# Optimization experiments

Measured on AMD Instinct MI355X. Metric: run time of the kernel, lower is better.

The kernel has to match this reference:

```python
import jax, jax.numpy as jnp
import numpy as np

N, E, G = 50000, 800000, 1000
F, FM, L, H, T = 128, 16, 7, 128, 12
DIN, DH = 2 * F + 1, 2 * (2 * F + 1)  # 257, 514
UIN, UH = F + FM, 2 * F               # 144, 256

def swish(x):
    return x * jax.nn.sigmoid(x)

def setup_inputs() -> dict:
    key = jax.random.key(0)
    ks = jax.random.split(key, 16)
    pos = jax.random.normal(ks[0], (N, 3), dtype=jnp.float32)
    zi = jax.random.randint(ks[1], (N,), 0, 5)
    z = jnp.array([1, 6, 7, 8, 9], dtype=jnp.int64)[zi]  # valid atomic numbers
    edge_index = jax.random.randint(ks[2], (2, E), 0, N)
    batch = jnp.sort(jax.random.randint(ks[3], (N,), 0, G))
    def w(k, shape, fan_in):
        return jax.random.normal(k, shape, dtype=jnp.float32) / np.sqrt(fan_in)
    return {
        'pos': pos, 'z': z, 'edge_index': edge_index, 'batch': batch,
        'emb': jax.random.normal(ks[4], (5, F), dtype=jnp.float32),
        'W_msg1': w(ks[5], (L, DIN, DH), DIN), 'b_msg1': jnp.zeros((L, DH), jnp.float32),
        'W_msg2': w(ks[6], (L, DH, FM), DH), 'b_msg2': jnp.zeros((L, FM), jnp.float32),
        'W_up1': w(ks[7], (L, UIN, UH), UIN), 'b_up1': jnp.zeros((L, UH), jnp.float32),
        'W_up2': w(ks[8], (L, UH, F), UH), 'b_up2': jnp.zeros((L, F), jnp.float32),
        'Wp1': w(ks[9], (F, H), F), 'bp1': jnp.zeros((H,), jnp.float32),
        'Wp2': w(ks[10], (H, H), H), 'bp2': jnp.zeros((H,), jnp.float32),
        'Wr1': w(ks[11], (H, H), H), 'br1': jnp.zeros((H,), jnp.float32),
        'Wr2': w(ks[12], (H, T), H), 'br2': jnp.zeros((T,), jnp.float32),
        'n_graphs': G,
    }

def reference(pos, z, edge_index, batch, emb, W_msg1, b_msg1, W_msg2, b_msg2,
              W_up1, b_up1, W_up2, b_up2, Wp1, bp1, Wp2, bp2, Wr1, br1, Wr2, br2,
              n_graphs):
    n = pos.shape[0]
    atomic = jnp.array([-1, 0, -1, -1, -1, -1, 1, 2, 3, 4])
    h = emb[atomic[z]]                                  # [N, F]
    src, dst = edge_index[0], edge_index[1]
    d = pos[src] - pos[dst]
    norm2 = jnp.sum(d * d, axis=1)                      # [E] squared distance
    for l in range(W_msg1.shape[0]):
        inp = jnp.concatenate([h[dst], h[src], norm2[:, None]], axis=1)  # x_i, x_j, norm2
        m = swish(inp @ W_msg1[l] + b_msg1[l])
        m = swish(m @ W_msg2[l] + b_msg2[l])            # [E, FM]
        agg = jax.ops.segment_sum(m, dst, num_segments=n)  # aggregate at target nodes
        u = jnp.concatenate([agg, h], axis=1)           # [N, F+FM]
        u = swish(u @ W_up1[l] + b_up1[l])
        h = u @ W_up2[l] + b_up2[l] + h                 # residual update
    proj = swish(h @ Wp1 + bp1) @ Wp2 + bp2             # node_proj
    pooled = jax.ops.segment_sum(proj, batch, num_segments=n_graphs)  # global_add_pool
    return swish(pooled @ Wr1 + br1) @ Wr2 + br2        # readout [G, T]
```

## Files before the change

### kernel.cpp

```cpp
#include <hip/hip_runtime.h>
#include <hip/hip_bf16.h>
#include <cstdint>
#include <cstddef>

typedef _Float16 h16x8 __attribute__((ext_vector_type(8)));
typedef float f32x4 __attribute__((ext_vector_type(4)));

#define NSTRIPE 2

__device__ __forceinline__ void splitf16(float v, _Float16& hi, _Float16& lo) {
    hi = (_Float16)v;
    lo = (_Float16)(v - (float)hi);
}
__device__ __forceinline__ float swish_fast(float x) {
    float e = __expf(-x);
    return x * __builtin_amdgcn_rcpf(1.0f + e);
}

__global__ void init_nodes(const int* __restrict__ z, const float* __restrict__ emb,
                           float* __restrict__ hf, _Float16* __restrict__ hhi,
                           _Float16* __restrict__ hlo, int N) {
    int tid = blockIdx.x * 256 + threadIdx.x;
    int n = tid >> 7, f = tid & 127;
    int zv = z[n];
    int idx5 = (zv == 1) ? 0 : (zv - 5);
    float v = emb[idx5 * 128 + f];
    hf[tid] = v;
    _Float16 hi, lo;
    splitf16(v, hi, lo);
    hhi[tid] = hi;
    hlo[tid] = lo;
}

__device__ __forceinline__ int edge_key(int d, int s, int N, int stripeSz) {
    return (d / stripeSz) * N + s;
}

__global__ void hist_kernel(const int* __restrict__ src, const int* __restrict__ dst,
                            int* __restrict__ hist, int E, int N, int stripeSz) {
    int e = blockIdx.x * 256 + threadIdx.x;
    if (e < E) atomicAdd(&hist[edge_key(dst[e], src[e], N, stripeSz)], 1);
}

__global__ void scan_p1(const int* __restrict__ hist, int* __restrict__ blocksum, int KN) {
    __shared__ int s[256];
    int idx = blockIdx.x * 256 + threadIdx.x;
    int v = (idx < KN) ? hist[idx] : 0;
    s[threadIdx.x] = v;
    __syncthreads();
    for (int d = 128; d > 0; d >>= 1) {
        if (threadIdx.x < d) s[threadIdx.x] += s[threadIdx.x + d];
        __syncthreads();
    }
    if (threadIdx.x == 0) blocksum[blockIdx.x] = s[0];
}

__global__ void scan_p2(int* __restrict__ blocksum, int NB) {
    __shared__ int s[1024];
    int t = threadIdx.x;
    int v = (t < NB) ? blocksum[t] : 0;
    s[t] = v;
    __syncthreads();
    for (int d = 1; d < 1024; d <<= 1) {
        int x = (t >= d) ? s[t - d] : 0;
        __syncthreads();
        s[t] += x;
        __syncthreads();
    }
    if (t < NB) blocksum[t] = s[t] - v;
}

__global__ void scan_p3(const int* __restrict__ hist, const int* __restrict__ blocksum,
                        int* __restrict__ cursor, int KN) {
    __shared__ int s[256];
    int idx = blockIdx.x * 256 + threadIdx.x;
    int v = (idx < KN) ? hist[idx] : 0;
    s[threadIdx.x] = v;
    __syncthreads();
    for (int d = 1; d < 256; d <<= 1) {
        int x = (threadIdx.x >= d) ? s[threadIdx.x - d] : 0;
        __syncthreads();
        s[threadIdx.x] += x;
        __syncthreads();
    }
    if (idx < KN) cursor[idx] = blocksum[blockIdx.x] + s[threadIdx.x] - v;
}

__global__ void scatter_kernel(const int* __restrict__ src, const int* __restrict__ dst,
                               int* __restrict__ cursor, int* __restrict__ perm,
                               int E, int N, int stripeSz) {
    int e = blockIdx.x * 256 + threadIdx.x;
    if (e < E) {
        int p = atomicAdd(&cursor[edge_key(dst[e], src[e], N, stripeSz)], 1);
        perm[p] = e;
    }
}

__global__ void reorder_kernel(const int* __restrict__ perm, const int* __restrict__ src,
                               const int* __restrict__ dst, const float* __restrict__ pos,
                               int* __restrict__ srcS, int* __restrict__ dstS,
                               float* __restrict__ n2S, int E) {
    int i = blockIdx.x * 256 + threadIdx.x;
    if (i >= E) return;
    int e = perm[i];
    int si = src[e], di = dst[e];
    srcS[i] = si;
    dstS[i] = di;
    float dx = pos[si * 3 + 0] - pos[di * 3 + 0];
    float dy = pos[si * 3 + 1] - pos[di * 3 + 1];
    float dz = pos[si * 3 + 2] - pos[di * 3 + 2];
    n2S[i] = dx * dx + dy * dy + dz * dz;
}

__global__ void pack_msg1(const float* __restrict__ Wm1, const float* __restrict__ bm1,
                          const float* __restrict__ Wm2,
                          _Float16* __restrict__ Bp1A, float* __restrict__ biasA,
                          _Float16* __restrict__ w1cA, _Float16* __restrict__ W2pA) {
    int l = blockIdx.y;
    const float* Wm1l = Wm1 + (size_t)l * 257 * 514;
    const float* bm1l = bm1 + (size_t)l * 514;
    const float* Wm2l = Wm2 + (size_t)l * 514 * 16;
    _Float16* Bp1 = Bp1A + (size_t)l * 139264;
    float* bias1088 = biasA + (size_t)l * 1088;
    _Float16* w1c = w1cA + (size_t)l * 544;
    _Float16* W2p = W2pA + (size_t)l * 8704;

    int t = blockIdx.x * 256 + threadIdx.x;
    int i = t & 7;
    int lane = (t >> 3) & 63;
    int rest = t >> 9;
    int cb = rest % 68;
    int ks = rest / 68;
    int k = ks * 32 + ((lane >> 4) << 3) + i;
    int ch = cb * 16 + (lane & 15);
    float val;
    if (ch < 544) {
        val = (ch < 514) ? Wm1l[k * 514 + ch] : 0.f;
    } else {
        int c = ch - 544;
        val = (c < 514) ? Wm1l[(128 + k) * 514 + c] : 0.f;
    }
    Bp1[t] = (_Float16)val;
    if (t < 1088) bias1088[t] = (t < 514) ? bm1l[t] : 0.f;
    if (t < 544) w1c[t] = (_Float16)((t < 514) ? Wm1l[256 * 514 + t] : 0.f);
    if (t < 8704) {
        int i2 = t & 7, lane2 = (t >> 3) & 63, ks2 = t >> 9;
        int k2 = ks2 * 32 + ((lane2 >> 4) << 3) + i2;
        int c2 = lane2 & 15;
        W2p[t] = (_Float16)((k2 < 514) ? Wm2l[k2 * 16 + c2] : 0.f);
    }
}

__global__ void pack_generic(const float* __restrict__ Wall, size_t strideW, int K, int Nc,
                             _Float16* __restrict__ BpAll, size_t strideB) {
    int l = blockIdx.y;
    const float* W = Wall + (size_t)l * strideW;
    _Float16* Bp = BpAll + (size_t)l * strideB;
    int t = blockIdx.x * 256 + threadIdx.x;
    int i = t & 7;
    int lane = (t >> 3) & 63;
    int rest = t >> 9;
    int CB = Nc >> 4;
    int cb = rest % CB;
    int ks = rest / CB;
    int k = ks * 32 + ((lane >> 4) << 3) + i;
    int c = cb * 16 + (lane & 15);
    float val = (k < K) ? W[(size_t)k * Nc + c] : 0.f;
    Bp[t] = (_Float16)val;
}

__global__ __launch_bounds__(256) void tab_gemm(
    const _Float16* __restrict__ Ahi,
    const _Float16* __restrict__ Bp, const float* __restrict__ bias,
    _Float16* __restrict__ TA, _Float16* __restrict__ TB, float* __restrict__ agg, int N) {
    {
        int base = blockIdx.x * 1024 + threadIdx.x;
#pragma unroll
        for (int q = 0; q < 4; ++q) {
            int idx = base + q * 256;
            if (idx < N * 16) agg[idx] = 0.f;
        }
    }
    int lane = threadIdx.x & 63;
    int wid = threadIdx.x >> 6;
    int row0 = blockIdx.x * 64 + wid * 16;
    if (row0 >= N) return;
    const size_t arow = (size_t)(row0 + (lane & 15)) * 128;
    const int ak = (lane >> 4) * 8;
    h16x8 ah[4];
#pragma unroll
    for (int ks = 0; ks < 4; ++ks)
        ah[ks] = *(const h16x8*)(Ahi + arow + ks * 32 + ak);
    int col16 = lane & 15;
    int rb = (lane >> 4) * 4;
    for (int cb = 0; cb < 68; ++cb) {
        f32x4 acc = {0.f, 0.f, 0.f, 0.f};
#pragma unroll
        for (int ks = 0; ks < 4; ++ks) {
            h16x8 bh = *(const h16x8*)(Bp + ((size_t)(ks * 68 + cb) * 64 + lane) * 8);
            acc = __builtin_amdgcn_mfma_f32_16x16x32_f16(ah[ks], bh, acc, 0, 0, 0);
        }
        int col = cb * 16 + col16;
        float bv = bias[col];
        if (cb < 34) {
#pragma unroll
            for (int i = 0; i < 4; ++i)
                TA[(size_t)(row0 + rb + i) * 544 + col] = (_Float16)(acc[i] + bv);
        } else {
#pragma unroll
            for (int i = 0; i < 4; ++i)
                TB[(size_t)(row0 + rb + i) * 544 + (col - 544)] = (_Float16)(acc[i] + bv);
        }
    }
}

template <int KS, int CB, int MODE>
__global__ __launch_bounds__(256) void gemmA(
    const _Float16* __restrict__ Ahi, const _Float16* __restrict__ Alo, int lda,
    const _Float16* __restrict__ Bp, const float* __restrict__ bias,
    _Float16* __restrict__ outB, _Float16* __restrict__ outB2, int ldoB,
    const int* __restrict__ batch, float* __restrict__ pooled, int N) {
    int lane = threadIdx.x & 63;
    int wid = threadIdx.x >> 6;
    int row0 = blockIdx.x * 64 + wid * 16;
    if (row0 >= N) return;
    const size_t arow = (size_t)(row0 + (lane & 15)) * lda;
    const int ak = (lane >> 4) * 8;
    h16x8 ah[KS], al[KS];
#pragma unroll
    for (int ks = 0; ks < KS; ++ks) {
        ah[ks] = *(const h16x8*)(Ahi + arow + ks * 32 + ak);
        al[ks] = *(const h16x8*)(Alo + arow + ks * 32 + ak);
    }
    int col16 = lane & 15;
    int rb = (lane >> 4) * 4;
    for (int cb = 0; cb < CB; ++cb) {
        f32x4 acc = {0.f, 0.f, 0.f, 0.f};
#pragma unroll
        for (int ks = 0; ks < KS; ++ks) {
            h16x8 bh = *(const h16x8*)(Bp + ((size_t)(ks * CB + cb) * 64 + lane) * 8);
            acc = __builtin_amdgcn_mfma_f32_16x16x32_f16(ah[ks], bh, acc, 0, 0, 0);
            acc = __builtin_amdgcn_mfma_f32_16x16x32_f16(al[ks], bh, acc, 0, 0, 0);
        }
        int col = cb * 16 + col16;
        float bv = bias[col];
#pragma unroll
        for (int i = 0; i < 4; ++i) {
            int row = row0 + rb + i;
            float v = acc[i] + bv;
            if (MODE == 1) {
                float s = swish_fast(v);
                _Float16 hi, lo;
                splitf16(s, hi, lo);
                outB[(size_t)row * ldoB + col] = hi;
                outB2[(size_t)row * ldoB + col] = lo;
            } else {
                unsafeAtomicAdd(&pooled[(size_t)batch[row] * 128 + col], v);
            }
        }
    }
}

__global__ __launch_bounds__(256) void up_fused(
    const float* __restrict__ agg, const _Float16* __restrict__ Bp1,
    const float* __restrict__ b1, const _Float16* __restrict__ Bp2,
    const float* __restrict__ b2,
    float* __restrict__ hf, _Float16* __restrict__ hhi, _Float16* __restrict__ hlo, int N) {
    __shared__ _Float16 sUh[4][16][264];
    __shared__ _Float16 sUl[4][16][264];
    int lane = threadIdx.x & 63;
    int wid = threadIdx.x >> 6;
    int row0 = blockIdx.x * 64 + wid * 16;
    if (row0 >= N) return;
    int r = row0 + (lane & 15);
    const int ak = (lane >> 4) * 8;
    h16x8 ah[5], al[5];
#pragma unroll
    for (int ks = 0; ks < 5; ++ks) {
        int c0 = ks * 32 + ak;
        f32x4 v0, v1;
        if (c0 < 16) {
            v0 = *(const f32x4*)(agg + (size_t)r * 16 + c0);
            v1 = *(const f32x4*)(agg + (size_t)r * 16 + c0 + 4);
        } else if (c0 < 144) {
            v0 = *(const f32x4*)(hf + (size_t)r * 128 + c0 - 16);
            v1 = *(const f32x4*)(hf + (size_t)r * 128 + c0 - 12);
        } else {
            v0 = f32x4{0.f, 0.f, 0.f, 0.f};
            v1 = f32x4{0.f, 0.f, 0.f, 0.f};
        }
        h16x8 hi8, lo8;
#pragma unroll
        for (int jj = 0; jj < 8; ++jj) {
            float x = (jj < 4) ? v0[jj] : v1[jj - 4];
            _Float16 h, l;
            splitf16(x, h, l);
            hi8[jj] = h;
            lo8[jj] = l;
        }
        ah[ks] = hi8;
        al[ks] = lo8;
    }
    int col16 = lane & 15;
    int rb = (lane >> 4) * 4;
    for (int cb = 0; cb < 16; ++cb) {
        f32x4 acc = {0.f, 0.f, 0.f, 0.f};
#pragma unroll
        for (int ks = 0; ks < 5; ++ks) {
            h16x8 bh = *(const h16x8*)(Bp1 + ((size_t)(ks * 16 + cb) * 64 + lane) * 8);
            acc = __builtin_amdgcn_mfma_f32_16x16x32_f16(ah[ks], bh, acc, 0, 0, 0);
            acc = __builtin_amdgcn_mfma_f32_16x16x32_f16(al[ks], bh, acc, 0, 0, 0);
        }
        int col = cb * 16 + col16;
        float bv = b1[col];
#pragma unroll
        for (int i = 0; i < 4; ++i) {
            float s = swish_fast(acc[i] + bv);
            _Float16 hi, lo;
            splitf16(s, hi, lo);
            sUh[wid][rb + i][col] = hi;
            sUl[wid][rb + i][col] = lo;
        }
    }
    __syncthreads();
    h16x8 ah2[8], al2[8];
#pragma unroll
    for (int ks = 0; ks < 8; ++ks) {
        ah2[ks] = *(const h16x8*)(&sUh[wid][lane & 15][ks * 32 + ak]);
        al2[ks] = *(const h16x8*)(&sUl[wid][lane & 15][ks * 32 + ak]);
    }
    for (int cb = 0; cb < 8; ++cb) {
        f32x4 acc = {0.f, 0.f, 0.f, 0.f};
#pragma unroll
        for (int ks = 0; ks < 8; ++ks) {
            h16x8 bh = *(const h16x8*)(Bp2 + ((size_t)(ks * 8 + cb) * 64 + lane) * 8);
            acc = __builtin_amdgcn_mfma_f32_16x16x32_f16(ah2[ks], bh, acc, 0, 0, 0);
            acc = __builtin_amdgcn_mfma_f32_16x16x32_f16(al2[ks], bh, acc, 0, 0, 0);
        }
        int col = cb * 16 + col16;
        float bv = b2[col];
#pragma unroll
        for (int i = 0; i < 4; ++i) {
            int row = row0 + rb + i;
            float h = acc[i] + bv + hf[(size_t)row * 128 + col];
            hf[(size_t)row * 128 + col] = h;
            _Float16 hi, lo;
            splitf16(h, hi, lo);
            hhi[(size_t)row * 128 + col] = hi;
            hlo[(size_t)row * 128 + col] = lo;
        }
    }
}

__global__ __launch_bounds__(256) void edge_kernel(
    const _Float16* __restrict__ TA, const _Float16* __restrict__ TB,
    const _Float16* __restrict__ w1c, const _Float16* __restrict__ W2p,
    const float* __restrict__ bm2l,
    const int* __restrict__ srcS, const int* __restrict__ dstS,
    const float* __restrict__ n2S, float* __restrict__ agg) {
    __shared__ _Float16 sW[8704];
    __shared__ _Float16 sw1[544];
    for (int t = threadIdx.x; t < 1088; t += 256)
        ((h16x8*)sW)[t] = ((const h16x8*)W2p)[t];
    for (int t = threadIdx.x; t < 544; t += 256) sw1[t] = w1c[t];
    __syncthreads();

    int lane = threadIdx.x & 63;
    int wid = threadIdx.x >> 6;
    int ebase = blockIdx.x * 128 + wid * 32;
    int rr = lane & 15;
    int e0 = ebase + rr;
    int e1 = ebase + 16 + rr;
    int di0 = dstS[e0], si0 = srcS[e0];
    int di1 = dstS[e1], si1 = srcS[e1];
    _Float16 n20 = (_Float16)n2S[e0];
    _Float16 n21 = (_Float16)n2S[e1];
    const int ak = (lane >> 4) * 8;
    const _Float16* pa0 = TA + (size_t)di0 * 544 + ak;
    const _Float16* pb0 = TB + (size_t)si0 * 544 + ak;
    const _Float16* pa1 = TA + (size_t)di1 * 544 + ak;
    const _Float16* pb1 = TB + (size_t)si1 * 544 + ak;

    const _Float16 nl2e = (_Float16)(-1.44269504f);
    f32x4 acc0 = {0.f, 0.f, 0.f, 0.f};
    f32x4 acc1 = {0.f, 0.f, 0.f, 0.f};

    h16x8 bufA[16], bufB[16], bufT[4];

    auto issue4 = [&](h16x8* buf, int K) {
#pragma unroll
        for (int q = 0; q < 4; ++q) {
            buf[q * 4 + 0] = *(const h16x8*)(pa0 + (K + q) * 32);
            buf[q * 4 + 1] = *(const h16x8*)(pb0 + (K + q) * 32);
            buf[q * 4 + 2] = *(const h16x8*)(pa1 + (K + q) * 32);
            buf[q * 4 + 3] = *(const h16x8*)(pb1 + (K + q) * 32);
        }
    };
    auto step = [&](const h16x8* buf, int q, int ks) {
        h16x8 va0 = buf[q * 4 + 0], vb0 = buf[q * 4 + 1];
        h16x8 va1 = buf[q * 4 + 2], vb1 = buf[q * 4 + 3];
        h16x8 wv = *(const h16x8*)(sw1 + ks * 32 + ak);
        h16x8 x0 = va0 + vb0 + wv * n20;
        h16x8 ev0 = __builtin_elementwise_exp2(x0 * nl2e);
        h16x8 d0 = ev0 + (_Float16)1.0f;
        h16x8 r0;
#pragma unroll
        for (int j = 0; j < 8; ++j) r0[j] = __builtin_amdgcn_rcph(d0[j]);
        h16x8 m0 = x0 * r0;
        h16x8 x1 = va1 + vb1 + wv * n21;
        h16x8 ev1 = __builtin_elementwise_exp2(x1 * nl2e);
        h16x8 d1 = ev1 + (_Float16)1.0f;
        h16x8 r1;
#pragma unroll
        for (int j = 0; j < 8; ++j) r1[j] = __builtin_amdgcn_rcph(d1[j]);
        h16x8 m1 = x1 * r1;
        h16x8 bh = *(const h16x8*)(sW + (ks * 64 + lane) * 8);
        acc0 = __builtin_amdgcn_mfma_f32_16x16x32_f16(m0, bh, acc0, 0, 0, 0);
        acc1 = __builtin_amdgcn_mfma_f32_16x16x32_f16(m1, bh, acc1, 0, 0, 0);
    };

    issue4(bufA, 0);
    __builtin_amdgcn_sched_barrier(0);
    issue4(bufB, 4);
    __builtin_amdgcn_sched_barrier(0);
#pragma unroll
    for (int q = 0; q < 4; ++q) step(bufA, q, q);
    issue4(bufA, 8);
    __builtin_amdgcn_sched_barrier(0);
#pragma unroll
    for (int q = 0; q < 4; ++q) step(bufB, q, 4 + q);
    issue4(bufB, 12);
    __builtin_amdgcn_sched_barrier(0);
#pragma unroll
    for (int q = 0; q < 4; ++q) step(bufA, q, 8 + q);
    bufT[0] = *(const h16x8*)(pa0 + 16 * 32);
    bufT[1] = *(const h16x8*)(pb0 + 16 * 32);
    bufT[2] = *(const h16x8*)(pa1 + 16 * 32);
    bufT[3] = *(const h16x8*)(pb1 + 16 * 32);
    __builtin_amdgcn_sched_barrier(0);
#pragma unroll
    for (int q = 0; q < 4; ++q) step(bufB, q, 12 + q);
    step(bufT, 0, 16);

    int col = lane & 15;
    float b2 = bm2l[col];
#pragma unroll
    for (int i = 0; i < 4; ++i) {
        int ea = ebase + (lane >> 4) * 4 + i;
        float v0 = swish_fast(acc0[i] + b2);
        unsafeAtomicAdd(&agg[(size_t)dstS[ea] * 16 + col], v0);
        int eb = ea + 16;
        float v1 = swish_fast(acc1[i] + b2);
        unsafeAtomicAdd(&agg[(size_t)dstS[eb] * 16 + col], v1);
    }
}

__global__ void readout(const float* __restrict__ pooled, const float* __restrict__ Wr1,
                        const float* __restrict__ br1, const float* __restrict__ Wr2,
                        const float* __restrict__ br2, float* __restrict__ out) {
    __shared__ float row[128];
    __shared__ float tt[128];
    int g = blockIdx.x;
    int t = threadIdx.x;
    row[t] = pooled[g * 128 + t];
    __syncthreads();
    float s = br1[t];
    for (int k = 0; k < 128; ++k) s += row[k] * Wr1[k * 128 + t];
    tt[t] = swish_fast(s);
    __syncthreads();
    if (t < 12) {
        float o = br2[t];
        for (int j = 0; j < 128; ++j) o += tt[j] * Wr2[j * 12 + t];
        out[g * 12 + t] = o;
    }
}

extern "C" void kernel_launch(void* const* d_in, const int* in_sizes, int n_in,
                              void* d_out, int out_size, void* d_ws, size_t ws_size,
                              hipStream_t stream) {
    const float* pos = (const float*)d_in[0];
    const int* z = (const int*)d_in[1];
    const int* ei = (const int*)d_in[2];
    const int* batch = (const int*)d_in[3];
    const float* emb = (const float*)d_in[4];
    const float* Wm1 = (const float*)d_in[5];
    const float* bm1 = (const float*)d_in[6];
    const float* Wm2 = (const float*)d_in[7];
    const float* bm2 = (const float*)d_in[8];
    const float* Wu1 = (const float*)d_in[9];
    const float* bu1 = (const float*)d_in[10];
    const float* Wu2 = (const float*)d_in[11];
    const float* bu2 = (const float*)d_in[12];
    const float* Wp1 = (const float*)d_in[13];
    const float* bp1v = (const float*)d_in[14];
    const float* Wp2 = (const float*)d_in[15];
    const float* bp2v = (const float*)d_in[16];
    const float* Wr1 = (const float*)d_in[17];
    const float* br1 = (const float*)d_in[18];
    const float* Wr2 = (const float*)d_in[19];
    const float* br2 = (const float*)d_in[20];

    const int N = in_sizes[0] / 3;
    const int E = in_sizes[2] / 2;
    const int G = out_size / 12;
    const int* src = ei;
    const int* dstp = ei + E;
    const int stripeSz = (N + NSTRIPE - 1) / NSTRIPE;
    const int KN = NSTRIPE * N;
    const int NB = (KN + 255) / 256;

    char* ws = (char*)d_ws;
    size_t off = 0;
    auto alloc = [&](size_t bytes) -> char* {
        char* p = ws + off;
        off += (bytes + 255) & ~(size_t)255;
        return p;
    };
    _Float16* TA = (_Float16*)alloc((size_t)N * 544 * 2);
    _Float16* TB = (_Float16*)alloc((size_t)N * 544 * 2);
    float* hf = (float*)alloc((size_t)N * 128 * 4);
    _Float16* hhi = (_Float16*)alloc((size_t)N * 128 * 2);
    _Float16* hlo = (_Float16*)alloc((size_t)N * 128 * 2);
    float* agg = (float*)alloc((size_t)N * 16 * 4);
    float* pooled = (float*)alloc((size_t)G * 128 * 4);
    int* hist = (int*)alloc((size_t)KN * 4);
    int* cursor = (int*)alloc((size_t)KN * 4);
    int* blocksum = (int*)alloc((size_t)NB * 4);
    int* perm = (int*)alloc((size_t)E * 4);
    int* srcS = (int*)alloc((size_t)E * 4);
    int* dstS = (int*)alloc((size_t)E * 4);
    float* n2S = (float*)alloc((size_t)E * 4);
    _Float16* Bp1A = (_Float16*)alloc((size_t)7 * 139264 * 2);
    float* biasA = (float*)alloc((size_t)7 * 1088 * 4);
    _Float16* w1cA = (_Float16*)alloc((size_t)7 * 544 * 2);
    _Float16* W2pA = (_Float16*)alloc((size_t)7 * 8704 * 2);
    _Float16* BpU1A = (_Float16*)alloc((size_t)7 * 40960 * 2);
    _Float16* BpU2A = (_Float16*)alloc((size_t)7 * 32768 * 2);
    _Float16* BpP1 = (_Float16*)alloc(16384 * 2);
    _Float16* BpP2 = (_Float16*)alloc(16384 * 2);

    _Float16* t1hi = TB;
    _Float16* t1lo = TB + (size_t)N * 128;

    init_nodes<<<(N * 128) / 256, 256, 0, stream>>>(z, emb, hf, hhi, hlo, N);

    hipMemsetAsync(hist, 0, (size_t)KN * 4, stream);
    hist_kernel<<<(E + 255) / 256, 256, 0, stream>>>(src, dstp, hist, E, N, stripeSz);
    scan_p1<<<NB, 256, 0, stream>>>(hist, blocksum, KN);
    scan_p2<<<1, 1024, 0, stream>>>(blocksum, NB);
    scan_p3<<<NB, 256, 0, stream>>>(hist, blocksum, cursor, KN);
    scatter_kernel<<<(E + 255) / 256, 256, 0, stream>>>(src, dstp, cursor, perm, E, N, stripeSz);
    reorder_kernel<<<(E + 255) / 256, 256, 0, stream>>>(perm, src, dstp, pos, srcS, dstS, n2S, E);

    pack_msg1<<<dim3(139264 / 256, 7), 256, 0, stream>>>(Wm1, bm1, Wm2, Bp1A, biasA, w1cA, W2pA);
    pack_generic<<<dim3(160, 7), 256, 0, stream>>>(Wu1, (size_t)144 * 256, 144, 256, BpU1A, 40960);
    pack_generic<<<dim3(128, 7), 256, 0, stream>>>(Wu2, (size_t)256 * 128, 256, 128, BpU2A, 32768);
    pack_generic<<<dim3(64, 1), 256, 0, stream>>>(Wp1, 0, 128, 128, BpP1, 0);
    pack_generic<<<dim3(64, 1), 256, 0, stream>>>(Wp2, 0, 128, 128, BpP2, 0);

    const int gA = (N + 63) / 64;
    for (int l = 0; l < 7; ++l) {
        tab_gemm<<<gA, 256, 0, stream>>>(hhi, Bp1A + (size_t)l * 139264,
                                         biasA + (size_t)l * 1088, TA, TB, agg, N);
        edge_kernel<<<E / 128, 256, 0, stream>>>(TA, TB, w1cA + (size_t)l * 544,
                                                 W2pA + (size_t)l * 8704, bm2 + l * 16,
                                                 srcS, dstS, n2S, agg);
        up_fused<<<gA, 256, 0, stream>>>(agg, BpU1A + (size_t)l * 40960, bu1 + l * 256,
                                         BpU2A + (size_t)l * 32768, bu2 + l * 128,
                                         hf, hhi, hlo, N);
    }

    gemmA<4, 8, 1><<<gA, 256, 0, stream>>>(
        hhi, hlo, 128, BpP1, bp1v,
        t1hi, t1lo, 128, nullptr, nullptr, N);
    hipMemsetAsync(pooled, 0, (size_t)G * 128 * 4, stream);
    gemmA<4, 8, 3><<<gA, 256, 0, stream>>>(
        t1hi, t1lo, 128, BpP2, bp2v,
        nullptr, nullptr, 0, batch, pooled, N);
    readout<<<G, 128, 0, stream>>>(pooled, Wr1, br1, Wr2, br2, (float*)d_out);
}
```

Measured before the change: 2.054 ms.

## Fuse node update with next layer's table GEMM and final projection-pool

Each layer's node-update kernel now also computes the next layer's per-node message tables (TA/TB) straight from shared memory. It also zeroes the aggregation buffer, so the separate tab_gemm launches are gone. The last layer's update instead runs the two projection GEMMs and atomically pools the result, replacing the gemmA kernels and the hhi/hlo round-trips through global memory. This cuts launches and global traffic for the node features, but makes each block longer and heavier on registers.

```diff
diff --git a/kernel.cpp b/kernel.cpp
--- a/kernel.cpp
+++ b/kernel.cpp
@@ -18,18 +18,14 @@
 }
 
 __global__ void init_nodes(const int* __restrict__ z, const float* __restrict__ emb,
-                           float* __restrict__ hf, _Float16* __restrict__ hhi,
-                           _Float16* __restrict__ hlo, int N) {
+                           float* __restrict__ hf, _Float16* __restrict__ hhi, int N) {
     int tid = blockIdx.x * 256 + threadIdx.x;
     int n = tid >> 7, f = tid & 127;
     int zv = z[n];
     int idx5 = (zv == 1) ? 0 : (zv - 5);
     float v = emb[idx5 * 128 + f];
     hf[tid] = v;
-    _Float16 hi, lo;
-    splitf16(v, hi, lo);
-    hhi[tid] = hi;
-    hlo[tid] = lo;
+    hhi[tid] = (_Float16)v;
 }
 
 __device__ __forceinline__ int edge_key(int d, int s, int N, int stripeSz) {
@@ -214,121 +210,90 @@
     }
 }
 
-template <int KS, int CB, int MODE>
-__global__ __launch_bounds__(256) void gemmA(
-    const _Float16* __restrict__ Ahi, const _Float16* __restrict__ Alo, int lda,
-    const _Float16* __restrict__ Bp, const float* __restrict__ bias,
-    _Float16* __restrict__ outB, _Float16* __restrict__ outB2, int ldoB,
+template <int MODE>
+__global__ __launch_bounds__(256) void up_combo(
+    const float* __restrict__ agg, float* __restrict__ hf,
+    const _Float16* __restrict__ Bp1, const float* __restrict__ b1,
+    const _Float16* __restrict__ Bp2, const float* __restrict__ b2,
+    const _Float16* __restrict__ BpX1, const float* __restrict__ bX1,
+    const _Float16* __restrict__ BpX2, const float* __restrict__ bX2,
+    _Float16* __restrict__ TA, _Float16* __restrict__ TB, float* __restrict__ aggz,
     const int* __restrict__ batch, float* __restrict__ pooled, int N) {
+    __shared__ _Float16 sA[4][16][272];
+    __shared__ _Float16 sB[4][16][272];
     int lane = threadIdx.x & 63;
     int wid = threadIdx.x >> 6;
     int row0 = blockIdx.x * 64 + wid * 16;
-    if (row0 >= N) return;
-    const size_t arow = (size_t)(row0 + (lane & 15)) * lda;
-    const int ak = (lane >> 4) * 8;
-    h16x8 ah[KS], al[KS];
-#pragma unroll
-    for (int ks = 0; ks < KS; ++ks) {
-        ah[ks] = *(const h16x8*)(Ahi + arow + ks * 32 + ak);
-        al[ks] = *(const h16x8*)(Alo + arow + ks * 32 + ak);
-    }
     int col16 = lane & 15;
     int rb = (lane >> 4) * 4;
-    for (int cb = 0; cb < CB; ++cb) {
-        f32x4 acc = {0.f, 0.f, 0.f, 0.f};
-#pragma unroll
-        for (int ks = 0; ks < KS; ++ks) {
-            h16x8 bh = *(const h16x8*)(Bp + ((size_t)(ks * CB + cb) * 64 + lane) * 8);
-            acc = __builtin_amdgcn_mfma_f32_16x16x32_f16(ah[ks], bh, acc, 0, 0, 0);
-            acc = __builtin_amdgcn_mfma_f32_16x16x32_f16(al[ks], bh, acc, 0, 0, 0);
-        }
-        int col = cb * 16 + col16;
-        float bv = bias[col];
-#pragma unroll
-        for (int i = 0; i < 4; ++i) {
-            int row = row0 + rb + i;
-            float v = acc[i] + bv;
-            if (MODE == 1) {
-                float s = swish_fast(v);
+    const int ak = (lane >> 4) * 8;
+
+    if (row0 < N) {
+        int r = row0 + col16;
+        h16x8 ah[5], al[5];
+#pragma unroll
+        for (int ks = 0; ks < 5; ++ks) {
+            int c0 = ks * 32 + ak;
+            f32x4 v0, v1;
+            if (c0 < 16) {
+                v0 = *(const f32x4*)(agg + (size_t)r * 16 + c0);
+                v1 = *(const f32x4*)(agg + (size_t)r * 16 + c0 + 4);
+            } else if (c0 < 144) {
+                v0 = *(const f32x4*)(hf + (size_t)r * 128 + c0 - 16);
+                v1 = *(const f32x4*)(hf + (size_t)r * 128 + c0 - 12);
+            } else {
+                v0 = f32x4{0.f, 0.f, 0.f, 0.f};
+                v1 = f32x4{0.f, 0.f, 0.f, 0.f};
+            }
+            h16x8 hi8, lo8;
+#pragma unroll
+            for (int jj = 0; jj < 8; ++jj) {
+                float x = (jj < 4) ? v0[jj] : v1[jj - 4];
+                _Float16 h, l;
+                splitf16(x, h, l);
+                hi8[jj] = h;
+                lo8[jj] = l;
+            }
+            ah[ks] = hi8;
+            al[ks] = lo8;
+        }
+        for (int cb = 0; cb < 16; ++cb) {
+            f32x4 acc = {0.f, 0.f, 0.f, 0.f};
+#pragma unroll
+            for (int ks = 0; ks < 5; ++ks) {
+                h16x8 bh = *(const h16x8*)(Bp1 + ((size_t)(ks * 16 + cb) * 64 + lane) * 8);
+                acc = __builtin_amdgcn_mfma_f32_16x16x32_f16(ah[ks], bh, acc, 0, 0, 0);
+                acc = __builtin_amdgcn_mfma_f32_16x16x32_f16(al[ks], bh, acc, 0, 0, 0);
+            }
+            int col = cb * 16 + col16;
+            float bv = b1[col];
+#pragma unroll
+            for (int i = 0; i < 4; ++i) {
+                float s = swish_fast(acc[i] + bv);
                 _Float16 hi, lo;
                 splitf16(s, hi, lo);
-                outB[(size_t)row * ldoB + col] = hi;
-                outB2[(size_t)row * ldoB + col] = lo;
-            } else {
-                unsafeAtomicAdd(&pooled[(size_t)batch[row] * 128 + col], v);
-            }
-        }
-    }
-}
-
-__global__ __launch_bounds__(256) void up_fused(
-    const float* __restrict__ agg, const _Float16* __restrict__ Bp1,
-    const float* __restrict__ b1, const _Float16* __restrict__ Bp2,
-    const float* __restrict__ b2,
-    float* __restrict__ hf, _Float16* __restrict__ hhi, _Float16* __restrict__ hlo, int N) {
-    __shared__ _Float16 sUh[4][16][264];
-    __shared__ _Float16 sUl[4][16][264];
-    int lane = threadIdx.x & 63;
-    int wid = threadIdx.x >> 6;
-    int row0 = blockIdx.x * 64 + wid * 16;
+                sA[wid][rb + i][col] = hi;
+                sB[wid][rb + i][col] = lo;
+            }
+        }
+    }
+    __syncthreads();
+    if (MODE == 0) {
+        int base = blockIdx.x * 1024 + threadIdx.x;
+#pragma unroll
+        for (int q = 0; q < 4; ++q) {
+            int idx = base + q * 256;
+            if (idx < N * 16) aggz[idx] = 0.f;
+        }
+    }
     if (row0 >= N) return;
-    int r = row0 + (lane & 15);
-    const int ak = (lane >> 4) * 8;
-    h16x8 ah[5], al[5];
-#pragma unroll
-    for (int ks = 0; ks < 5; ++ks) {
-        int c0 = ks * 32 + ak;
-        f32x4 v0, v1;
-        if (c0 < 16) {
-            v0 = *(const f32x4*)(agg + (size_t)r * 16 + c0);
-            v1 = *(const f32x4*)(agg + (size_t)r * 16 + c0 + 4);
-        } else if (c0 < 144) {
-            v0 = *(const f32x4*)(hf + (size_t)r * 128 + c0 - 16);
-            v1 = *(const f32x4*)(hf + (size_t)r * 128 + c0 - 12);
-        } else {
-            v0 = f32x4{0.f, 0.f, 0.f, 0.f};
-            v1 = f32x4{0.f, 0.f, 0.f, 0.f};
-        }
-        h16x8 hi8, lo8;
-#pragma unroll
-        for (int jj = 0; jj < 8; ++jj) {
-            float x = (jj < 4) ? v0[jj] : v1[jj - 4];
-            _Float16 h, l;
-            splitf16(x, h, l);
-            hi8[jj] = h;
-            lo8[jj] = l;
-        }
-        ah[ks] = hi8;
-        al[ks] = lo8;
-    }
-    int col16 = lane & 15;
-    int rb = (lane >> 4) * 4;
-    for (int cb = 0; cb < 16; ++cb) {
-        f32x4 acc = {0.f, 0.f, 0.f, 0.f};
-#pragma unroll
-        for (int ks = 0; ks < 5; ++ks) {
-            h16x8 bh = *(const h16x8*)(Bp1 + ((size_t)(ks * 16 + cb) * 64 + lane) * 8);
-            acc = __builtin_amdgcn_mfma_f32_16x16x32_f16(ah[ks], bh, acc, 0, 0, 0);
-            acc = __builtin_amdgcn_mfma_f32_16x16x32_f16(al[ks], bh, acc, 0, 0, 0);
-        }
-        int col = cb * 16 + col16;
-        float bv = b1[col];
-#pragma unroll
-        for (int i = 0; i < 4; ++i) {
-            float s = swish_fast(acc[i] + bv);
-            _Float16 hi, lo;
-            splitf16(s, hi, lo);
-            sUh[wid][rb + i][col] = hi;
-            sUl[wid][rb + i][col] = lo;
-        }
-    }
-    __syncthreads();
     h16x8 ah2[8], al2[8];
 #pragma unroll
     for (int ks = 0; ks < 8; ++ks) {
-        ah2[ks] = *(const h16x8*)(&sUh[wid][lane & 15][ks * 32 + ak]);
-        al2[ks] = *(const h16x8*)(&sUl[wid][lane & 15][ks * 32 + ak]);
-    }
+        ah2[ks] = *(const h16x8*)(&sA[wid][col16][ks * 32 + ak]);
+        al2[ks] = *(const h16x8*)(&sB[wid][col16][ks * 32 + ak]);
+    }
+    __syncthreads();
     for (int cb = 0; cb < 8; ++cb) {
         f32x4 acc = {0.f, 0.f, 0.f, 0.f};
 #pragma unroll
@@ -343,11 +308,87 @@
         for (int i = 0; i < 4; ++i) {
             int row = row0 + rb + i;
             float h = acc[i] + bv + hf[(size_t)row * 128 + col];
-            hf[(size_t)row * 128 + col] = h;
+            if (MODE == 0) hf[(size_t)row * 128 + col] = h;
             _Float16 hi, lo;
             splitf16(h, hi, lo);
-            hhi[(size_t)row * 128 + col] = hi;
-            hlo[(size_t)row * 128 + col] = lo;
+            sA[wid][rb + i][col] = hi;
+            if (MODE == 1) sB[wid][rb + i][col] = lo;
+        }
+    }
+    __syncthreads();
+    if (MODE == 0) {
+        h16x8 ah3[4];
+#pragma unroll
+        for (int ks = 0; ks < 4; ++ks)
+            ah3[ks] = *(const h16x8*)(&sA[wid][col16][ks * 32 + ak]);
+        for (int cb = 0; cb < 68; ++cb) {
+            f32x4 acc = {0.f, 0.f, 0.f, 0.f};
+#pragma unroll
+            for (int ks = 0; ks < 4; ++ks) {
+                h16x8 bh = *(const h16x8*)(BpX1 + ((size_t)(ks * 68 + cb) * 64 + lane) * 8);
+                acc = __builtin_amdgcn_mfma_f32_16x16x32_f16(ah3[ks], bh, acc, 0, 0, 0);
+            }
+            int col = cb * 16 + col16;
+            float bv = bX1[col];
+            if (cb < 34) {
+#pragma unroll
+                for (int i = 0; i < 4; ++i)
+                    TA[(size_t)(row0 + rb + i) * 544 + col] = (_Float16)(acc[i] + bv);
+            } else {
+#pragma unroll
+                for (int i = 0; i < 4; ++i)
+                    TB[(size_t)(row0 + rb + i) * 544 + (col - 544)] = (_Float16)(acc[i] + bv);
+            }
+        }
+    } else {
+        h16x8 ah3[4], al3[4];
+#pragma unroll
+        for (int ks = 0; ks < 4; ++ks) {
+            ah3[ks] = *(const h16x8*)(&sA[wid][col16][ks * 32 + ak]);
+            al3[ks] = *(const h16x8*)(&sB[wid][col16][ks * 32 + ak]);
+        }
+        __syncthreads();
+        for (int cb = 0; cb < 8; ++cb) {
+            f32x4 acc = {0.f, 0.f, 0.f, 0.f};
+#pragma unroll
+            for (int ks = 0; ks < 4; ++ks) {
+                h16x8 bh = *(const h16x8*)(BpX1 + ((size_t)(ks * 8 + cb) * 64 + lane) * 8);
+                acc = __builtin_amdgcn_mfma_f32_16x16x32_f16(ah3[ks], bh, acc, 0, 0, 0);
+                acc = __builtin_amdgcn_mfma_f32_16x16x32_f16(al3[ks], bh, acc, 0, 0, 0);
+            }
+            int col = cb * 16 + col16;
+            float bv = bX1[col];
+#pragma unroll
+            for (int i = 0; i < 4; ++i) {
+                float s = swish_fast(acc[i] + bv);
+                _Float16 hi, lo;
+                splitf16(s, hi, lo);
+                sA[wid][rb + i][col] = hi;
+                sB[wid][rb + i][col] = lo;
+            }
+        }
+        __syncthreads();
+        h16x8 ah4[4], al4[4];
+#pragma unroll
+        for (int ks = 0; ks < 4; ++ks) {
+            ah4[ks] = *(const h16x8*)(&sA[wid][col16][ks * 32 + ak]);
+            al4[ks] = *(const h16x8*)(&sB[wid][col16][ks * 32 + ak]);
+        }
+        for (int cb = 0; cb < 8; ++cb) {
+            f32x4 acc = {0.f, 0.f, 0.f, 0.f};
+#pragma unroll
+            for (int ks = 0; ks < 4; ++ks) {
+                h16x8 bh = *(const h16x8*)(BpX2 + ((size_t)(ks * 8 + cb) * 64 + lane) * 8);
+                acc = __builtin_amdgcn_mfma_f32_16x16x32_f16(ah4[ks], bh, acc, 0, 0, 0);
+                acc = __builtin_amdgcn_mfma_f32_16x16x32_f16(al4[ks], bh, acc, 0, 0, 0);
+            }
+            int col = cb * 16 + col16;
+            float bv = bX2[col];
+#pragma unroll
+            for (int i = 0; i < 4; ++i) {
+                int row = row0 + rb + i;
+                unsafeAtomicAdd(&pooled[(size_t)batch[row] * 128 + col], acc[i] + bv);
+            }
         }
     }
 }
@@ -520,7 +561,6 @@
     _Float16* TB = (_Float16*)alloc((size_t)N * 544 * 2);
     float* hf = (float*)alloc((size_t)N * 128 * 4);
     _Float16* hhi = (_Float16*)alloc((size_t)N * 128 * 2);
-    _Float16* hlo = (_Float16*)alloc((size_t)N * 128 * 2);
     float* agg = (float*)alloc((size_t)N * 16 * 4);
     float* pooled = (float*)alloc((size_t)G * 128 * 4);
     int* hist = (int*)alloc((size_t)KN * 4);
@@ -539,10 +579,7 @@
     _Float16* BpP1 = (_Float16*)alloc(16384 * 2);
     _Float16* BpP2 = (_Float16*)alloc(16384 * 2);
 
-    _Float16* t1hi = TB;
-    _Float16* t1lo = TB + (size_t)N * 128;
-
-    init_nodes<<<(N * 128) / 256, 256, 0, stream>>>(z, emb, hf, hhi, hlo, N);
+    init_nodes<<<(N * 128) / 256, 256, 0, stream>>>(z, emb, hf, hhi, N);
 
     hipMemsetAsync(hist, 0, (size_t)KN * 4, stream);
     hist_kernel<<<(E + 255) / 256, 256, 0, stream>>>(src, dstp, hist, E, N, stripeSz);
@@ -557,25 +594,27 @@
     pack_generic<<<dim3(128, 7), 256, 0, stream>>>(Wu2, (size_t)256 * 128, 256, 128, BpU2A, 32768);
     pack_generic<<<dim3(64, 1), 256, 0, stream>>>(Wp1, 0, 128, 128, BpP1, 0);
     pack_generic<<<dim3(64, 1), 256, 0, stream>>>(Wp2, 0, 128, 128, BpP2, 0);
+    hipMemsetAsync(pooled, 0, (size_t)G * 128 * 4, stream);
 
     const int gA = (N + 63) / 64;
+    tab_gemm<<<gA, 256, 0, stream>>>(hhi, Bp1A, biasA, TA, TB, agg, N);
     for (int l = 0; l < 7; ++l) {
-        tab_gemm<<<gA, 256, 0, stream>>>(hhi, Bp1A + (size_t)l * 139264,
-                                         biasA + (size_t)l * 1088, TA, TB, agg, N);
         edge_kernel<<<E / 128, 256, 0, stream>>>(TA, TB, w1cA + (size_t)l * 544,
                                                  W2pA + (size_t)l * 8704, bm2 + l * 16,
                                                  srcS, dstS, n2S, agg);
-        up_fused<<<gA, 256, 0, stream>>>(agg, BpU1A + (size_t)l * 40960, bu1 + l * 256,
-                                         BpU2A + (size_t)l * 32768, bu2 + l * 128,
-                                         hf, hhi, hlo, N);
-    }
-
-    gemmA<4, 8, 1><<<gA, 256, 0, stream>>>(
-        hhi, hlo, 128, BpP1, bp1v,
-        t1hi, t1lo, 128, nullptr, nullptr, N);
-    hipMemsetAsync(pooled, 0, (size_t)G * 128 * 4, stream);
-    gemmA<4, 8, 3><<<gA, 256, 0, stream>>>(
-        t1hi, t1lo, 128, BpP2, bp2v,
-        nullptr, nullptr, 0, batch, pooled, N);
+        if (l < 6) {
+            up_combo<0><<<gA, 256, 0, stream>>>(
+                agg, hf, BpU1A + (size_t)l * 40960, bu1 + l * 256,
+                BpU2A + (size_t)l * 32768, bu2 + l * 128,
+                Bp1A + (size_t)(l + 1) * 139264, biasA + (size_t)(l + 1) * 1088,
+                nullptr, nullptr, TA, TB, agg, nullptr, nullptr, N);
+        } else {
+            up_combo<1><<<gA, 256, 0, stream>>>(
+                agg, hf, BpU1A + (size_t)l * 40960, bu1 + l * 256,
+                BpU2A + (size_t)l * 32768, bu2 + l * 128,
+                BpP1, bp1v, BpP2, bp2v,
+                nullptr, nullptr, nullptr, batch, pooled, N);
+        }
+    }
     readout<<<G, 128, 0, stream>>>(pooled, Wr1, br1, Wr2, br2, (float*)d_out);
 }
```

New measurement: 2.190 ms. 1.07x slower.
